# Kernel optimization log

Hardware: AMD Instinct MI355X
Metric: run time of the kernel (lower is better)

Reference implementation:

```python
import jax, jax.numpy as jnp
import numpy as np

ALPHA = 0.2  # leaky relu slope
NEG_INF = -9e15  # matches torch constant -9000000000000000.0


def setup_inputs() -> dict:
    key = jax.random.key(0)
    k1, k2, k3, k4, k5 = jax.random.split(key, 5)
    B, S, FIN, FOUT, H = 1, 4096, 128, 64, 8
    input_seq = jax.random.normal(k1, (B, S, FIN), dtype=jnp.float32)
    adj = jax.random.randint(k2, (B, S, S), 0, 2, dtype=jnp.int32)
    W = jax.random.normal(k3, (H, FIN, FOUT), dtype=jnp.float32) * 0.1
    a_1 = jax.random.normal(k4, (H, FOUT, 1), dtype=jnp.float32) * 0.1
    a_2 = jax.random.normal(k5, (H, FOUT, 1), dtype=jnp.float32) * 0.1
    return {"input_seq": input_seq, "adj": adj, "W": W, "a_1": a_1, "a_2": a_2}


def reference(input_seq, adj, W, a_1, a_2):
    B, S, _ = input_seq.shape
    H, _, FOUT = W.shape
    # h: [B, H, S, FOUT]
    h = jnp.einsum('bni,hio->bhno', input_seq, W)
    f1 = jnp.einsum('bhno,hoz->bhnz', h, a_1)[..., 0]  # [B,H,S]
    f2 = jnp.einsum('bhno,hoz->bhnz', h, a_2)[..., 0]  # [B,H,S]
    # e[b,h,i,j] = f1[i] + f2[j]
    e = jax.nn.leaky_relu(f1[:, :, :, None] + f2[:, :, None, :], ALPHA)
    mask = adj[:, None, :, :] > 0  # [B,1,S,S] broadcast over heads
    e = jnp.where(mask, e, NEG_INF)
    # NOTE: original softmax is over dim=2 (source-node axis), not -1
    attention = jax.nn.softmax(e, axis=2)
    # dropout is inference-mode no-op
    node_out = jnp.einsum('bhij,bhjo->bhio', attention, h)  # [B,H,S,FOUT]
    node_out = jnp.transpose(node_out, (0, 2, 1, 3)).reshape(B, S, H * FOUT)
    node_out = jax.nn.elu(node_out)
    return jnp.squeeze(node_out)
```

## Files before the change

### kernel.cpp

```cpp
#include <hip/hip_runtime.h>

#define S 4096
#define PS 4128
#define FIN 128
#define FOUT 64
#define H 8
#define ALPHA 0.2f

typedef __attribute__((ext_vector_type(2)))  _Float16 f16x2;
typedef __attribute__((ext_vector_type(8)))  _Float16 f16x8;
typedef __attribute__((ext_vector_type(16))) float    f32x16;

__device__ __forceinline__ unsigned short f2h(float x) {
    return __builtin_bit_cast(unsigned short, (_Float16)x);
}

__global__ __launch_bounds__(256) void k_proj(const float* __restrict__ X,
                                              const float* __restrict__ W,
                                              const float* __restrict__ a1,
                                              const float* __restrict__ a2,
                                              unsigned short* __restrict__ hT,
                                              float2* __restrict__ E1h,
                                              float2* __restrict__ E2p) {
    __shared__ float xs[64][36];
    __shared__ float Ws[32][68];
    const int h  = blockIdx.y;
    const int j0 = blockIdx.x * 64;
    const int t  = threadIdx.x;
    const int fg = t & 15, rg = t >> 4;
    const int jr = t >> 2, q = t & 3;
    const int kw = t >> 3, cw = t & 7;
    float acc[4][4] = {};
#pragma unroll
    for (int k0 = 0; k0 < FIN; k0 += 32) {
        *(float4*)&xs[jr][q * 8]      = *(const float4*)&X[(j0 + jr) * FIN + k0 + q * 8];
        *(float4*)&xs[jr][q * 8 + 4]  = *(const float4*)&X[(j0 + jr) * FIN + k0 + q * 8 + 4];
        *(float4*)&Ws[kw][cw * 8]     = *(const float4*)&W[(h * FIN + k0 + kw) * FOUT + cw * 8];
        *(float4*)&Ws[kw][cw * 8 + 4] = *(const float4*)&W[(h * FIN + k0 + kw) * FOUT + cw * 8 + 4];
        __syncthreads();
#pragma unroll
        for (int kc = 0; kc < 8; ++kc) {
            float4 xr[4], wr[4];
#pragma unroll
            for (int r = 0; r < 4; ++r) xr[r] = *(const float4*)&xs[4 * rg + r][kc * 4];
#pragma unroll
            for (int kk = 0; kk < 4; ++kk) wr[kk] = *(const float4*)&Ws[kc * 4 + kk][fg * 4];
#pragma unroll
            for (int r = 0; r < 4; ++r) {
                const float* xp = (const float*)&xr[r];
#pragma unroll
                for (int kk = 0; kk < 4; ++kk) {
                    const float xv = xp[kk];
                    acc[r][0] += xv * wr[kk].x;
                    acc[r][1] += xv * wr[kk].y;
                    acc[r][2] += xv * wr[kk].z;
                    acc[r][3] += xv * wr[kk].w;
                }
            }
        }
        __syncthreads();
    }
    const float4 a1v = *(const float4*)&a1[h * FOUT + fg * 4];
    const float4 a2v = *(const float4*)&a2[h * FOUT + fg * 4];
#pragma unroll
    for (int r = 0; r < 4; ++r) {
        float p1 = acc[r][0] * a1v.x + acc[r][1] * a1v.y + acc[r][2] * a1v.z + acc[r][3] * a1v.w;
        float p2 = acc[r][0] * a2v.x + acc[r][1] * a2v.y + acc[r][2] * a2v.z + acc[r][3] * a2v.w;
#pragma unroll
        for (int off = 1; off < 16; off <<= 1) {
            p1 += __shfl_xor(p1, off, 64);
            p2 += __shfl_xor(p2, off, 64);
        }
        if (fg == 0) {
            const int row = j0 + 4 * rg + r;
            E1h[(size_t)row * H + h] = make_float2(__expf(p1), __expf(ALPHA * p1));
            E2p[h * S + row]         = make_float2(__expf(p2), __expf(ALPHA * p2));
        }
    }
#pragma unroll
    for (int c = 0; c < 4; ++c) {
        ushort4 pk;
        pk.x = f2h(acc[0][c]);
        pk.y = f2h(acc[1][c]);
        pk.z = f2h(acc[2][c]);
        pk.w = f2h(acc[3][c]);
        *(ushort4*)&hT[(size_t)(h * FOUT + fg * 4 + c) * PS + j0 + 4 * rg] = pk;
    }
}

__global__ __launch_bounds__(256) void k_colsum(const int* __restrict__ adj,
                                                const float2* __restrict__ E1h,
                                                const float2* __restrict__ E2p,
                                                float* __restrict__ Dpart,
                                                unsigned int* __restrict__ bmT) {
    __shared__ float red[4][H][64];
    const int j0    = blockIdx.x * 64;
    const int ibase = blockIdx.y * 256;
    const int t  = threadIdx.x;
    const int jl = t & 63;
    const int wv = __builtin_amdgcn_readfirstlane(t >> 6);
    float2 e2v[H];
    float Dl[H];
#pragma unroll
    for (int hh = 0; hh < H; ++hh) { e2v[hh] = E2p[hh * S + j0 + jl]; Dl[hh] = 0.f; }
    const int rowbase = ibase + wv * 64;
    for (int s = 0; s < 64; ++s) {
        const int row = rowbase + s;
        const float2* __restrict__ e1r = E1h + (size_t)row * H;
        const int av = adj[(size_t)row * S + j0 + jl];
        const unsigned long long blt = __ballot(av != 0);
        if (jl == 0) {
            bmT[(j0 >> 5) * S + row]       = (unsigned int)blt;
            bmT[((j0 >> 5) + 1) * S + row] = (unsigned int)(blt >> 32);
        }
        const float bf = av != 0 ? 1.f : 0.f;
#pragma unroll
        for (int hh = 0; hh < H; ++hh) {
            const float2 e1 = e1r[hh];
            Dl[hh] = fmaf(bf, fmaxf(e1.x * e2v[hh].x, e1.y * e2v[hh].y), Dl[hh]);
        }
    }
#pragma unroll
    for (int hh = 0; hh < H; ++hh) red[wv][hh][jl] = Dl[hh];
    __syncthreads();
    if (wv == 0) {
#pragma unroll
        for (int hh = 0; hh < H; ++hh) {
            const float sum = red[0][hh][jl] + red[1][hh][jl] +
                              red[2][hh][jl] + red[3][hh][jl];
            Dpart[(blockIdx.y * H + hh) * S + j0 + jl] = sum;
        }
    }
}

__global__ __launch_bounds__(512, 4) void k_attn(const unsigned int* __restrict__ bmT,
                                                 const float2* __restrict__ E1h,
                                                 const float* __restrict__ Dpart,
                                                 const float2* __restrict__ E2p,
                                                 const unsigned short* __restrict__ hT,
                                                 float* __restrict__ out) {
    __shared__ __align__(16) char smem[53248];
    const int h  = blockIdx.y;
    const int i0 = blockIdx.x * 64;
    const int t  = threadIdx.x;

    uint2* wE2s = (uint2*)smem;
#pragma unroll
    for (int u = 0; u < 4; ++u) {
        const int pair = t * 4 + u;
        const int j = 2 * pair;
        float sx = 0.f, sy = 0.f;
#pragma unroll
        for (int z = 0; z < 16; ++z) {
            const float2 d = *(const float2*)&Dpart[(z * H + h) * S + j];
            sx += d.x; sy += d.y;
        }
        const float4 e2 = *(const float4*)&E2p[h * S + j];
        const float wa = 1.0f / sx, wb = 1.0f / sy;
        f16x2 qx, qy;
        qx[0] = (_Float16)(e2.x * wa); qx[1] = (_Float16)(e2.z * wb);
        qy[0] = (_Float16)(e2.y * wa); qy[1] = (_Float16)(e2.w * wb);
        wE2s[pair] = make_uint2(__builtin_bit_cast(unsigned int, qx),
                                __builtin_bit_cast(unsigned int, qy));
    }
    __syncthreads();

    const int lane = t & 63, wv = t >> 6;
    const int q = wv >> 1, mw = wv & 1;
    const int am = lane & 31, kh = lane >> 5;
    const int i  = i0 + mw * 32 + am;
    const int jbase = q * 1024;

    const float2 e1 = E1h[(size_t)i * H + h];
    f16x2 ea2, eb2;
    ea2[0] = ea2[1] = (_Float16)e1.x;
    eb2[0] = eb2[1] = (_Float16)e1.y;

    f32x16 acc0 = {0,0,0,0,0,0,0,0,0,0,0,0,0,0,0,0};
    f32x16 acc1 = {0,0,0,0,0,0,0,0,0,0,0,0,0,0,0,0};

    const unsigned short* b0p = hT + (size_t)(h * FOUT + am) * PS + jbase;
    const unsigned short* b1p = hT + (size_t)(h * FOUT + am + 32) * PS + jbase;
    const unsigned int* bmcol = bmT + (jbase >> 5) * S + i;
    const uint2* e2s = wE2s + (jbase >> 1) + kh * 4;
    const unsigned int sh = kh * 8;

    for (int jt = 0; jt < 16; ++jt) {
        const unsigned int w0 = bmcol[(2 * jt) * S];
        const unsigned int w1 = bmcol[(2 * jt + 1) * S];
        unsigned int bys[4];
        bys[0] = (w0 >> sh) & 0xffu;
        bys[1] = (w0 >> (sh + 16)) & 0xffu;
        bys[2] = (w1 >> sh) & 0xffu;
        bys[3] = (w1 >> (sh + 16)) & 0xffu;
#pragma unroll
        for (int s = 0; s < 4; ++s) {
            const int ko = jt * 64 + s * 16 + kh * 8;
            const f16x8 b0 = *(const f16x8*)(b0p + ko);
            const f16x8 b1 = *(const f16x8*)(b1p + ko);
            const uint4 eA = *(const uint4*)(e2s + jt * 32 + s * 8);
            const uint4 eB = *(const uint4*)(e2s + jt * 32 + s * 8 + 2);
            const unsigned int by = bys[s];
            uint4 aw;
#define GAT_PAIR(pp, qxu, qyu, dst)                                               \
            {                                                                     \
                const f16x2 pa = ea2 * __builtin_bit_cast(f16x2, qxu);            \
                const f16x2 pb = eb2 * __builtin_bit_cast(f16x2, qyu);            \
                const unsigned int pm = __builtin_bit_cast(unsigned int,          \
                    __builtin_elementwise_max(pa, pb));                           \
                const unsigned int t2 = (by >> (2 * pp)) & 3u;                    \
                const unsigned int msk = ((0u - (t2 & 1u)) & 0xFFFFu) |           \
                                         ((0u - (t2 >> 1)) << 16);                \
                dst = pm & msk;                                                   \
            }
            GAT_PAIR(0, eA.x, eA.y, aw.x)
            GAT_PAIR(1, eA.z, eA.w, aw.y)
            GAT_PAIR(2, eB.x, eB.y, aw.z)
            GAT_PAIR(3, eB.z, eB.w, aw.w)
#undef GAT_PAIR
            const f16x8 a = __builtin_bit_cast(f16x8, aw);
            acc0 = __builtin_amdgcn_mfma_f32_32x32x16_f16(a, b0, acc0, 0, 0, 0);
            acc1 = __builtin_amdgcn_mfma_f32_32x32x16_f16(a, b1, acc1, 0, 0, 0);
        }
    }
    __syncthreads();

    float* r1 = (float*)(smem + 16384);
    float* r3 = (float*)(smem + 16384 + 18432);
    const int ro = (mw * 64 + lane) * 36;
    if (q == 1) {
#pragma unroll
        for (int r = 0; r < 16; ++r) { r1[ro + r] = acc0[r]; r1[ro + 16 + r] = acc1[r]; }
    }
    if (q == 3) {
#pragma unroll
        for (int r = 0; r < 16; ++r) { r3[ro + r] = acc0[r]; r3[ro + 16 + r] = acc1[r]; }
    }
    __syncthreads();
    if (q == 0) {
#pragma unroll
        for (int r = 0; r < 16; ++r) { acc0[r] += r1[ro + r]; acc1[r] += r1[ro + 16 + r]; }
    }
    if (q == 2) {
#pragma unroll
        for (int r = 0; r < 16; ++r) { acc0[r] += r3[ro + r]; acc1[r] += r3[ro + 16 + r]; }
    }
    __syncthreads();
    if (q == 2) {
#pragma unroll
        for (int r = 0; r < 16; ++r) { r1[ro + r] = acc0[r]; r1[ro + 16 + r] = acc1[r]; }
    }
    __syncthreads();
    if (q == 0) {
#pragma unroll
        for (int r = 0; r < 16; ++r) { acc0[r] += r1[ro + r]; acc1[r] += r1[ro + 16 + r]; }
#pragma unroll
        for (int r = 0; r < 16; ++r) {
            const int il  = (r & 3) + 8 * (r >> 2) + 4 * kh;
            const int row = i0 + mw * 32 + il;
            const float x0 = acc0[r], x1 = acc1[r];
            out[row * (H * FOUT) + h * FOUT + am]      = x0 > 0.f ? x0 : __expf(x0) - 1.f;
            out[row * (H * FOUT) + h * FOUT + 32 + am] = x1 > 0.f ? x1 : __expf(x1) - 1.f;
        }
    }
}

extern "C" void kernel_launch(void* const* d_in, const int* in_sizes, int n_in,
                              void* d_out, int out_size, void* d_ws, size_t ws_size,
                              hipStream_t stream) {
    const float* X   = (const float*)d_in[0];
    const int*   adj = (const int*)d_in[1];
    const float* W   = (const float*)d_in[2];
    const float* a1  = (const float*)d_in[3];
    const float* a2  = (const float*)d_in[4];
    float* out = (float*)d_out;

    char* ws = (char*)d_ws;
    unsigned short* hT   = (unsigned short*)ws;
    float2*         E1h  = (float2*)(ws + 4325376);
    float2*         E2p  = (float2*)(ws + 4587520);
    float*          Dpart= (float*)(ws + 4849664);
    unsigned int*   bmT  = (unsigned int*)(ws + 6946816);

    k_proj  <<<dim3(S / 64, H),       256, 0, stream>>>(X, W, a1, a2, hT, E1h, E2p);
    k_colsum<<<dim3(S / 64, S / 256), 256, 0, stream>>>(adj, E1h, E2p, Dpart, bmT);
    k_attn  <<<dim3(S / 64, H),       512, 0, stream>>>(bmT, E1h, Dpart, E2p, hT, out);
}
```

Baseline: 211.2 us.

## Split attention over key halves, precompute normalized weights, add ELU reduce kernel

Moves the column-sum normalization of E2 out of the attention kernel into a separate k_finish kernel, so each attention block stops redundantly summing 16 Dpart partials. The attention grid gains a z dimension that splits the j range in two, which doubles the number of blocks and halves the per-block loop. Shared memory per block drops and launch bounds are raised to allow more resident blocks. The cost is writing and re-reading two partial output buffers and finishing with a separate k_elu kernel, plus two extra launches.

```diff
diff --git a/kernel.cpp b/kernel.cpp
--- a/kernel.cpp
+++ b/kernel.cpp
@@ -133,43 +133,47 @@
     }
 }
 
-__global__ __launch_bounds__(512, 4) void k_attn(const unsigned int* __restrict__ bmT,
+__global__ __launch_bounds__(256) void k_finish(const float* __restrict__ Dpart,
+                                                const float2* __restrict__ E2p,
+                                                uint2* __restrict__ wE2h) {
+    const int idx = blockIdx.x * 256 + threadIdx.x;
+    const int hh = idx >> 11, pp = idx & 2047;
+    const int j = 2 * pp;
+    float sx = 0.f, sy = 0.f;
+#pragma unroll
+    for (int z = 0; z < 16; ++z) {
+        const float2 d = *(const float2*)&Dpart[(z * H + hh) * S + j];
+        sx += d.x; sy += d.y;
+    }
+    const float4 e2 = *(const float4*)&E2p[hh * S + j];
+    const float wa = 1.0f / sx, wb = 1.0f / sy;
+    f16x2 qx, qy;
+    qx[0] = (_Float16)(e2.x * wa); qx[1] = (_Float16)(e2.z * wb);
+    qy[0] = (_Float16)(e2.y * wa); qy[1] = (_Float16)(e2.w * wb);
+    wE2h[idx] = make_uint2(__builtin_bit_cast(unsigned int, qx),
+                           __builtin_bit_cast(unsigned int, qy));
+}
+
+__global__ __launch_bounds__(512, 6) void k_attn(const unsigned int* __restrict__ bmT,
                                                  const float2* __restrict__ E1h,
-                                                 const float* __restrict__ Dpart,
-                                                 const float2* __restrict__ E2p,
+                                                 const uint2* __restrict__ wE2h,
                                                  const unsigned short* __restrict__ hT,
-                                                 float* __restrict__ out) {
-    __shared__ __align__(16) char smem[53248];
+                                                 float* __restrict__ outp) {
+    __shared__ __align__(16) char smem[36864];
     const int h  = blockIdx.y;
     const int i0 = blockIdx.x * 64;
+    const int z  = blockIdx.z;
     const int t  = threadIdx.x;
 
     uint2* wE2s = (uint2*)smem;
-#pragma unroll
-    for (int u = 0; u < 4; ++u) {
-        const int pair = t * 4 + u;
-        const int j = 2 * pair;
-        float sx = 0.f, sy = 0.f;
-#pragma unroll
-        for (int z = 0; z < 16; ++z) {
-            const float2 d = *(const float2*)&Dpart[(z * H + h) * S + j];
-            sx += d.x; sy += d.y;
-        }
-        const float4 e2 = *(const float4*)&E2p[h * S + j];
-        const float wa = 1.0f / sx, wb = 1.0f / sy;
-        f16x2 qx, qy;
-        qx[0] = (_Float16)(e2.x * wa); qx[1] = (_Float16)(e2.z * wb);
-        qy[0] = (_Float16)(e2.y * wa); qy[1] = (_Float16)(e2.w * wb);
-        wE2s[pair] = make_uint2(__builtin_bit_cast(unsigned int, qx),
-                                __builtin_bit_cast(unsigned int, qy));
-    }
+    ((uint4*)wE2s)[t] = ((const uint4*)(wE2h + h * (S / 2) + z * 1024))[t];
     __syncthreads();
 
     const int lane = t & 63, wv = t >> 6;
     const int q = wv >> 1, mw = wv & 1;
     const int am = lane & 31, kh = lane >> 5;
     const int i  = i0 + mw * 32 + am;
-    const int jbase = q * 1024;
+    const int jbase = z * 2048 + q * 512;
 
     const float2 e1 = E1h[(size_t)i * H + h];
     f16x2 ea2, eb2;
@@ -182,10 +186,10 @@
     const unsigned short* b0p = hT + (size_t)(h * FOUT + am) * PS + jbase;
     const unsigned short* b1p = hT + (size_t)(h * FOUT + am + 32) * PS + jbase;
     const unsigned int* bmcol = bmT + (jbase >> 5) * S + i;
-    const uint2* e2s = wE2s + (jbase >> 1) + kh * 4;
+    const uint2* e2s = wE2s + q * 256 + kh * 4;
     const unsigned int sh = kh * 8;
 
-    for (int jt = 0; jt < 16; ++jt) {
+    for (int jt = 0; jt < 8; ++jt) {
         const unsigned int w0 = bmcol[(2 * jt) * S];
         const unsigned int w1 = bmcol[(2 * jt + 1) * S];
         unsigned int bys[4];
@@ -225,8 +229,8 @@
     }
     __syncthreads();
 
-    float* r1 = (float*)(smem + 16384);
-    float* r3 = (float*)(smem + 16384 + 18432);
+    float* r1 = (float*)smem;
+    float* r3 = (float*)(smem + 18432);
     const int ro = (mw * 64 + lane) * 36;
     if (q == 1) {
 #pragma unroll
@@ -254,15 +258,29 @@
     if (q == 0) {
 #pragma unroll
         for (int r = 0; r < 16; ++r) { acc0[r] += r1[ro + r]; acc1[r] += r1[ro + 16 + r]; }
+        float* dst = outp + (size_t)z * (S * H * FOUT);
 #pragma unroll
         for (int r = 0; r < 16; ++r) {
             const int il  = (r & 3) + 8 * (r >> 2) + 4 * kh;
             const int row = i0 + mw * 32 + il;
-            const float x0 = acc0[r], x1 = acc1[r];
-            out[row * (H * FOUT) + h * FOUT + am]      = x0 > 0.f ? x0 : __expf(x0) - 1.f;
-            out[row * (H * FOUT) + h * FOUT + 32 + am] = x1 > 0.f ? x1 : __expf(x1) - 1.f;
-        }
-    }
+            dst[row * (H * FOUT) + h * FOUT + am]      = acc0[r];
+            dst[row * (H * FOUT) + h * FOUT + 32 + am] = acc1[r];
+        }
+    }
+}
+
+__global__ __launch_bounds__(256) void k_elu(const float* __restrict__ outp,
+                                             float* __restrict__ out) {
+    const int idx = (blockIdx.x * 256 + threadIdx.x) * 4;
+    const float4 p0 = *(const float4*)&outp[idx];
+    const float4 p1 = *(const float4*)&outp[S * H * FOUT + idx];
+    float4 v;
+    v.x = p0.x + p1.x; v.y = p0.y + p1.y; v.z = p0.z + p1.z; v.w = p0.w + p1.w;
+    v.x = v.x > 0.f ? v.x : __expf(v.x) - 1.f;
+    v.y = v.y > 0.f ? v.y : __expf(v.y) - 1.f;
+    v.z = v.z > 0.f ? v.z : __expf(v.z) - 1.f;
+    v.w = v.w > 0.f ? v.w : __expf(v.w) - 1.f;
+    *(float4*)&out[idx] = v;
 }
 
 extern "C" void kernel_launch(void* const* d_in, const int* in_sizes, int n_in,
@@ -281,8 +299,12 @@
     float2*         E2p  = (float2*)(ws + 4587520);
     float*          Dpart= (float*)(ws + 4849664);
     unsigned int*   bmT  = (unsigned int*)(ws + 6946816);
+    uint2*          wE2h = (uint2*)(ws + 9043968);
+    float*          outp = (float*)(ws + 9175040);
 
     k_proj  <<<dim3(S / 64, H),       256, 0, stream>>>(X, W, a1, a2, hT, E1h, E2p);
     k_colsum<<<dim3(S / 64, S / 256), 256, 0, stream>>>(adj, E1h, E2p, Dpart, bmT);
-    k_attn  <<<dim3(S / 64, H),       512, 0, stream>>>(bmT, E1h, Dpart, E2p, hT, out);
-}
+    k_finish<<<dim3(H * S / 512),     256, 0, stream>>>(Dpart, E2p, wE2h);
+    k_attn  <<<dim3(S / 64, H, 2),    512, 0, stream>>>(bmT, E1h, wE2h, hT, outp);
+    k_elu   <<<dim3(S * H * FOUT / 1024), 256, 0, stream>>>(outp, out);
+}
```

After: 209.6 us. About the same (-0.8%).
